# Kernel optimization log

Measured on AMD Instinct MI355X. Metric: run time of the kernel, lower is better.

The kernel has to match this reference:

```python
import jax, jax.numpy as jnp
import numpy as np

RADIUS = 2  # matches LGA(radius=2)


def setup_inputs() -> dict:
    key = jax.random.key(0)
    k1, k2 = jax.random.split(key)
    N, C, H, W = 4, 32, 384, 768
    K = 2 * RADIUS + 1
    input1 = jax.random.normal(k1, (N, C, H, W), dtype=jnp.float32)
    input2 = jax.random.uniform(k2, (N, K * K, H, W), dtype=jnp.float32)
    return {"input1": input1, "input2": input2}


def reference(input1, input2):
    # Local Guided Aggregation (GANet LGA):
    # out[n,c,h,w] = sum_{i,j in (2r+1)^2} input1[n,c,h+i-r,w+j-r] * input2[n,i*K+j,h,w]
    # Per-pixel 5x5 filter shared across channels; zero padding at borders.
    r = RADIUS
    K = 2 * r + 1
    N, C, H, W = input1.shape
    padded = jnp.pad(input1, ((0, 0), (0, 0), (r, r), (r, r)))
    out = jnp.zeros_like(input1)
    for i in range(K):
        for j in range(K):
            # shifted window [N,C,H,W] times per-pixel tap weight [N,1,H,W]
            out = out + padded[:, :, i:i + H, j:j + W] * input2[:, i * K + j][:, None, :, :]
    return out
```

## Files before the change

### kernel.cpp

```cpp
#include <hip/hip_runtime.h>


#define N_DIM 4
#define C_DIM 32
#define H_DIM 384
#define W_DIM 768
#define TH 4
#define TW 256
#define LROWS (TH + 4)
#define LW 260

__global__ __launch_bounds__(256, 3)
void lga_kernel(const float* __restrict__ in1,
                const float* __restrict__ in2,
                float* __restrict__ out) {
    __shared__ float lds[LROWS * LW];

    const int tid = threadIdx.x;
    const int tx  = tid & 63;
    const int ty  = tid >> 6;
    const int w0  = blockIdx.x * TW;
    const int h0  = blockIdx.y * TH;
    const int n   = blockIdx.z;

    const int h   = h0 + ty;
    const int wb  = w0 + 4 * tx;

    float4 wt[25];
    const float* w_src = in2 + ((size_t)n * 25) * (H_DIM * W_DIM)
                             + (size_t)h * W_DIM + wb;
#pragma unroll
    for (int t = 0; t < 25; ++t) {
        wt[t] = *(const float4*)(w_src + (size_t)t * (H_DIM * W_DIM));
    }

    const float* in1_n = in1 + (size_t)n * C_DIM * H_DIM * W_DIM;
    float*       out_n = out + (size_t)n * C_DIM * H_DIM * W_DIM;

    for (int c = 0; c < C_DIM; ++c) {
        const float* src = in1_n + (size_t)c * (H_DIM * W_DIM);

        for (int idx = tid; idx < LROWS * 65; idx += 256) {
            const int row = idx / 65;
            const int c4  = idx - row * 65;
            const int gh  = h0 - 2 + row;
            const int g   = w0 - 2 + 4 * c4;
            float4 v;
            if ((unsigned)gh < H_DIM && g >= 0 && g + 3 < W_DIM) {
                const float* p = src + gh * W_DIM + g;
                const float2 a = *(const float2*)p;
                const float2 b = *(const float2*)(p + 2);
                v = make_float4(a.x, a.y, b.x, b.y);
            } else {
                const bool rok = (unsigned)gh < H_DIM;
                const float* prow = src + gh * W_DIM;
                v.x = (rok && (unsigned)(g + 0) < W_DIM) ? prow[g + 0] : 0.f;
                v.y = (rok && (unsigned)(g + 1) < W_DIM) ? prow[g + 1] : 0.f;
                v.z = (rok && (unsigned)(g + 2) < W_DIM) ? prow[g + 2] : 0.f;
                v.w = (rok && (unsigned)(g + 3) < W_DIM) ? prow[g + 3] : 0.f;
            }
            *(float4*)&lds[row * LW + 4 * c4] = v;
        }
        __syncthreads();

        float acc0 = 0.f, acc1 = 0.f, acc2 = 0.f, acc3 = 0.f;
#pragma unroll
        for (int i = 0; i < 5; ++i) {
            const float* lrow = &lds[(ty + i) * LW + 4 * tx];
            const float4 A = *(const float4*)lrow;
            const float4 B = *(const float4*)(lrow + 4);
            const float win[8] = {A.x, A.y, A.z, A.w, B.x, B.y, B.z, B.w};
#pragma unroll
            for (int j = 0; j < 5; ++j) {
                const float4 wv = wt[5 * i + j];
                acc0 += wv.x * win[j + 0];
                acc1 += wv.y * win[j + 1];
                acc2 += wv.z * win[j + 2];
                acc3 += wv.w * win[j + 3];
            }
        }

        *(float4*)(out_n + (size_t)c * (H_DIM * W_DIM) + (size_t)h * W_DIM + wb)
            = make_float4(acc0, acc1, acc2, acc3);
        __syncthreads();
    }
}

extern "C" void kernel_launch(void* const* d_in, const int* in_sizes, int n_in,
                              void* d_out, int out_size, void* d_ws, size_t ws_size,
                              hipStream_t stream) {
    const float* in1 = (const float*)d_in[0];
    const float* in2 = (const float*)d_in[1];
    float* out = (float*)d_out;
    dim3 grid(W_DIM / TW, H_DIM / TH, N_DIM);
    lga_kernel<<<grid, 256, 0, stream>>>(in1, in2, out);
}
```

Baseline: 455.2 us.

## Double-buffer LDS tiles and prefetch next channel into registers

Global loads for the next channel's input tile are issued into registers before the current channel's 5x5 compute, then written to a second LDS buffer. This leaves one barrier per channel instead of two and lets load latency overlap the FMA work. The per-thread chunk offsets and border predicates are now computed once, and an empty asm pins the weight loads. The cost is higher register and LDS use (two 8x260 float buffers), which could lower occupancy under launch_bounds(256,3).

After: 418.8 us. 1.09x faster.

```diff
diff --git a/kernel.cpp b/kernel.cpp
--- a/kernel.cpp
+++ b/kernel.cpp
@@ -5,16 +5,18 @@
 #define C_DIM 32
 #define H_DIM 384
 #define W_DIM 768
+#define HW (H_DIM * W_DIM)
 #define TH 4
 #define TW 256
 #define LROWS (TH + 4)
 #define LW 260
+#define CHUNKS (LROWS * 65)
 
 __global__ __launch_bounds__(256, 3)
 void lga_kernel(const float* __restrict__ in1,
                 const float* __restrict__ in2,
                 float* __restrict__ out) {
-    __shared__ float lds[LROWS * LW];
+    __shared__ float lds[2][LROWS * LW];
 
     const int tid = threadIdx.x;
     const int tx  = tid & 63;
@@ -23,50 +25,90 @@
     const int h0  = blockIdx.y * TH;
     const int n   = blockIdx.z;
 
-    const int h   = h0 + ty;
-    const int wb  = w0 + 4 * tx;
+    const int h  = h0 + ty;
+    const int wb = w0 + 4 * tx;
 
     float4 wt[25];
-    const float* w_src = in2 + ((size_t)n * 25) * (H_DIM * W_DIM)
-                             + (size_t)h * W_DIM + wb;
+    {
+        const float* w_src = in2 + ((size_t)n * 25) * HW + (size_t)h * W_DIM + wb;
 #pragma unroll
-    for (int t = 0; t < 25; ++t) {
-        wt[t] = *(const float4*)(w_src + (size_t)t * (H_DIM * W_DIM));
+        for (int t = 0; t < 25; ++t) {
+            float4 v = *(const float4*)(w_src + (size_t)t * HW);
+            asm volatile("" : "+v"(v.x), "+v"(v.y), "+v"(v.z), "+v"(v.w));
+            wt[t] = v;
+        }
     }
 
-    const float* in1_n = in1 + (size_t)n * C_DIM * H_DIM * W_DIM;
-    float*       out_n = out + (size_t)n * C_DIM * H_DIM * W_DIM;
+    const float* in1_n = in1 + (size_t)n * C_DIM * HW;
+    float*       out_n = out + (size_t)n * C_DIM * HW;
+
+    int  soff[3];
+    int  ldst[3];
+    int  gcol[3];
+    bool fast[3];
+    bool rok[3];
+    bool act[3];
+#pragma unroll
+    for (int k = 0; k < 3; ++k) {
+        const int idx = tid + 256 * k;
+        act[k] = (k < 2) || (tid < CHUNKS - 512);
+        const int row = idx / 65;
+        const int c4  = idx - row * 65;
+        const int gh  = h0 - 2 + row;
+        const int g   = w0 - 2 + 4 * c4;
+        rok[k]  = (unsigned)gh < H_DIM;
+        gcol[k] = g;
+        fast[k] = rok[k] && (g >= 0) && (g + 3 < W_DIM);
+        soff[k] = (rok[k] ? gh : 0) * W_DIM + g;
+        ldst[k] = row * LW + 4 * c4;
+    }
+
+    auto load_chunk = [&](const float* src, int k) -> float4 {
+        float4 v;
+        if (fast[k]) {
+            const float* p = src + soff[k];
+            const float2 a = *(const float2*)p;
+            const float2 b = *(const float2*)(p + 2);
+            v = make_float4(a.x, a.y, b.x, b.y);
+        } else {
+            const int g = gcol[k];
+            const float* prow = src + (soff[k] - g);
+            v.x = (rok[k] && (unsigned)(g + 0) < W_DIM) ? prow[g + 0] : 0.f;
+            v.y = (rok[k] && (unsigned)(g + 1) < W_DIM) ? prow[g + 1] : 0.f;
+            v.z = (rok[k] && (unsigned)(g + 2) < W_DIM) ? prow[g + 2] : 0.f;
+            v.w = (rok[k] && (unsigned)(g + 3) < W_DIM) ? prow[g + 3] : 0.f;
+        }
+        return v;
+    };
+
+    {
+        float4 v0 = load_chunk(in1_n, 0);
+        float4 v1 = load_chunk(in1_n, 1);
+        float4 v2 = make_float4(0.f, 0.f, 0.f, 0.f);
+        if (act[2]) v2 = load_chunk(in1_n, 2);
+        *(float4*)&lds[0][ldst[0]] = v0;
+        *(float4*)&lds[0][ldst[1]] = v1;
+        if (act[2]) *(float4*)&lds[0][ldst[2]] = v2;
+    }
+    __syncthreads();
 
     for (int c = 0; c < C_DIM; ++c) {
-        const float* src = in1_n + (size_t)c * (H_DIM * W_DIM);
+        const int  cur  = c & 1;
+        const bool more = (c + 1 < C_DIM);
 
-        for (int idx = tid; idx < LROWS * 65; idx += 256) {
-            const int row = idx / 65;
-            const int c4  = idx - row * 65;
-            const int gh  = h0 - 2 + row;
-            const int g   = w0 - 2 + 4 * c4;
-            float4 v;
-            if ((unsigned)gh < H_DIM && g >= 0 && g + 3 < W_DIM) {
-                const float* p = src + gh * W_DIM + g;
-                const float2 a = *(const float2*)p;
-                const float2 b = *(const float2*)(p + 2);
-                v = make_float4(a.x, a.y, b.x, b.y);
-            } else {
-                const bool rok = (unsigned)gh < H_DIM;
-                const float* prow = src + gh * W_DIM;
-                v.x = (rok && (unsigned)(g + 0) < W_DIM) ? prow[g + 0] : 0.f;
-                v.y = (rok && (unsigned)(g + 1) < W_DIM) ? prow[g + 1] : 0.f;
-                v.z = (rok && (unsigned)(g + 2) < W_DIM) ? prow[g + 2] : 0.f;
-                v.w = (rok && (unsigned)(g + 3) < W_DIM) ? prow[g + 3] : 0.f;
-            }
-            *(float4*)&lds[row * LW + 4 * c4] = v;
+        float4 n0, n1, n2 = make_float4(0.f, 0.f, 0.f, 0.f);
+        if (more) {
+            const float* src = in1_n + (size_t)(c + 1) * HW;
+            n0 = load_chunk(src, 0);
+            n1 = load_chunk(src, 1);
+            if (act[2]) n2 = load_chunk(src, 2);
         }
-        __syncthreads();
 
         float acc0 = 0.f, acc1 = 0.f, acc2 = 0.f, acc3 = 0.f;
+        const float* lbase = &lds[cur][0];
 #pragma unroll
         for (int i = 0; i < 5; ++i) {
-            const float* lrow = &lds[(ty + i) * LW + 4 * tx];
+            const float* lrow = lbase + (ty + i) * LW + 4 * tx;
             const float4 A = *(const float4*)lrow;
             const float4 B = *(const float4*)(lrow + 4);
             const float win[8] = {A.x, A.y, A.z, A.w, B.x, B.y, B.z, B.w};
@@ -80,9 +122,16 @@
             }
         }
 
-        *(float4*)(out_n + (size_t)c * (H_DIM * W_DIM) + (size_t)h * W_DIM + wb)
+        *(float4*)(out_n + (size_t)c * HW + (size_t)h * W_DIM + wb)
             = make_float4(acc0, acc1, acc2, acc3);
-        __syncthreads();
+
+        if (more) {
+            float* dst = &lds[cur ^ 1][0];
+            *(float4*)&dst[ldst[0]] = n0;
+            *(float4*)&dst[ldst[1]] = n1;
+            if (act[2]) *(float4*)&dst[ldst[2]] = n2;
+            __syncthreads();
+        }
     }
 }
 
```

## Replace LDS staging with direct global window loads and clamped padding masks

Applied to the files above, without the earlier changes.

Drops the per-channel shared-memory tile and the two barriers per channel. Each thread now reads its 5x8 input window straight from global memory, with row and column indices clamped at the borders. Zero padding is applied by masking the tap weights once up front instead of per load. The launch also switches to a 1D grid with a remapping of workgroup IDs across eight groups, likely to spread work over XCDs and improve L2 locality. This removes sync and LDS traffic but relies on L1/L2 caches to absorb the redundant overlapping row reads.

Result: slower. 854.5 us (+87.7%).

```diff
diff --git a/kernel.cpp b/kernel.cpp
--- a/kernel.cpp
+++ b/kernel.cpp
@@ -5,71 +5,72 @@
 #define C_DIM 32
 #define H_DIM 384
 #define W_DIM 768
+#define HW (H_DIM * W_DIM)
 #define TH 4
 #define TW 256
-#define LROWS (TH + 4)
-#define LW 260
+#define NWG (W_DIM / TW * (H_DIM / TH) * N_DIM)
 
 __global__ __launch_bounds__(256, 3)
 void lga_kernel(const float* __restrict__ in1,
                 const float* __restrict__ in2,
                 float* __restrict__ out) {
-    __shared__ float lds[LROWS * LW];
+    int wg = blockIdx.x;
+    wg = (wg & 7) * (NWG / 8) + (wg >> 3);
+    const int bx = wg % 3;
+    const int by = (wg / 3) % (H_DIM / TH);
+    const int n  = wg / (3 * (H_DIM / TH));
 
     const int tid = threadIdx.x;
     const int tx  = tid & 63;
     const int ty  = tid >> 6;
-    const int w0  = blockIdx.x * TW;
-    const int h0  = blockIdx.y * TH;
-    const int n   = blockIdx.z;
-
-    const int h   = h0 + ty;
-    const int wb  = w0 + 4 * tx;
+    const int h   = by * TH + ty;
+    const int wb  = bx * TW + 4 * tx;
 
     float4 wt[25];
-    const float* w_src = in2 + ((size_t)n * 25) * (H_DIM * W_DIM)
-                             + (size_t)h * W_DIM + wb;
+    {
+        const float* w_src = in2 + ((size_t)n * 25) * HW + (size_t)h * W_DIM + wb;
 #pragma unroll
-    for (int t = 0; t < 25; ++t) {
-        wt[t] = *(const float4*)(w_src + (size_t)t * (H_DIM * W_DIM));
+        for (int i = 0; i < 5; ++i) {
+            const bool rv = (unsigned)(h + i - 2) < H_DIM;
+#pragma unroll
+            for (int j = 0; j < 5; ++j) {
+                const int t = 5 * i + j;
+                float4 v = *(const float4*)(w_src + (size_t)t * HW);
+                v.x = (rv && (unsigned)(wb + 0 + j - 2) < W_DIM) ? v.x : 0.f;
+                v.y = (rv && (unsigned)(wb + 1 + j - 2) < W_DIM) ? v.y : 0.f;
+                v.z = (rv && (unsigned)(wb + 2 + j - 2) < W_DIM) ? v.z : 0.f;
+                v.w = (rv && (unsigned)(wb + 3 + j - 2) < W_DIM) ? v.w : 0.f;
+                asm volatile("" : "+v"(v.x), "+v"(v.y), "+v"(v.z), "+v"(v.w));
+                wt[t] = v;
+            }
+        }
     }
 
-    const float* in1_n = in1 + (size_t)n * C_DIM * H_DIM * W_DIM;
-    float*       out_n = out + (size_t)n * C_DIM * H_DIM * W_DIM;
+    int rowoff[5];
+#pragma unroll
+    for (int i = 0; i < 5; ++i) {
+        int gh = h + i - 2;
+        gh = gh < 0 ? 0 : (gh > H_DIM - 1 ? H_DIM - 1 : gh);
+        rowoff[i] = gh * W_DIM;
+    }
+    const int o0 = (wb == 0) ? 0 : (wb - 2);
+    const int o3 = (wb + 4 > W_DIM - 2) ? (W_DIM - 2) : (wb + 4);
 
+    const float* src = in1 + (size_t)n * C_DIM * HW;
+    float*       dst = out + (size_t)n * C_DIM * HW + (size_t)h * W_DIM + wb;
+
+#pragma unroll 1
     for (int c = 0; c < C_DIM; ++c) {
-        const float* src = in1_n + (size_t)c * (H_DIM * W_DIM);
-
-        for (int idx = tid; idx < LROWS * 65; idx += 256) {
-            const int row = idx / 65;
-            const int c4  = idx - row * 65;
-            const int gh  = h0 - 2 + row;
-            const int g   = w0 - 2 + 4 * c4;
-            float4 v;
-            if ((unsigned)gh < H_DIM && g >= 0 && g + 3 < W_DIM) {
-                const float* p = src + gh * W_DIM + g;
-                const float2 a = *(const float2*)p;
-                const float2 b = *(const float2*)(p + 2);
-                v = make_float4(a.x, a.y, b.x, b.y);
-            } else {
-                const bool rok = (unsigned)gh < H_DIM;
-                const float* prow = src + gh * W_DIM;
-                v.x = (rok && (unsigned)(g + 0) < W_DIM) ? prow[g + 0] : 0.f;
-                v.y = (rok && (unsigned)(g + 1) < W_DIM) ? prow[g + 1] : 0.f;
-                v.z = (rok && (unsigned)(g + 2) < W_DIM) ? prow[g + 2] : 0.f;
-                v.w = (rok && (unsigned)(g + 3) < W_DIM) ? prow[g + 3] : 0.f;
-            }
-            *(float4*)&lds[row * LW + 4 * c4] = v;
-        }
-        __syncthreads();
+        const float* p = src + (size_t)c * HW;
 
         float acc0 = 0.f, acc1 = 0.f, acc2 = 0.f, acc3 = 0.f;
 #pragma unroll
         for (int i = 0; i < 5; ++i) {
-            const float* lrow = &lds[(ty + i) * LW + 4 * tx];
-            const float4 A = *(const float4*)lrow;
-            const float4 B = *(const float4*)(lrow + 4);
-            const float win[8] = {A.x, A.y, A.z, A.w, B.x, B.y, B.z, B.w};
+            const float* pr = p + rowoff[i];
+            const float2 a0 = *(const float2*)(pr + o0);
+            const float4 m  = *(const float4*)(pr + wb);
+            const float2 b1 = *(const float2*)(pr + o3);
+            const float win[8] = {a0.x, a0.y, m.x, m.y, m.z, m.w, b1.x, b1.y};
 #pragma unroll
             for (int j = 0; j < 5; ++j) {
                 const float4 wv = wt[5 * i + j];
@@ -80,9 +81,7 @@
             }
         }
 
-        *(float4*)(out_n + (size_t)c * (H_DIM * W_DIM) + (size_t)h * W_DIM + wb)
-            = make_float4(acc0, acc1, acc2, acc3);
-        __syncthreads();
+        *(float4*)(dst + (size_t)c * HW) = make_float4(acc0, acc1, acc2, acc3);
     }
 }
 
@@ -92,6 +91,5 @@
     const float* in1 = (const float*)d_in[0];
     const float* in2 = (const float*)d_in[1];
     float* out = (float*)d_out;
-    dim3 grid(W_DIM / TW, H_DIM / TH, N_DIM);
-    lga_kernel<<<grid, 256, 0, stream>>>(in1, in2, out);
+    lga_kernel<<<dim3(NWG), 256, 0, stream>>>(in1, in2, out);
 }
```
